# Optimization experiments

Hardware: AMD Instinct MI355X
Metric: run time of the kernel (lower is better)

The kernel has to match this reference:

```python
import jax, jax.numpy as jnp
import numpy as np


def setup_inputs() -> dict:
    key = jax.random.key(0)
    kx, ks = jax.random.split(key)
    X = jax.random.normal(kx, (8, 4096, 16), dtype=jnp.float32)
    # nn.Parameter(torch.rand(1) + 1.0)
    sigma = jax.random.uniform(ks, (1,), dtype=jnp.float32) + 1.0
    return {"X": X, "sigma": sigma}


def reference(X, sigma):
    sq = jnp.sum(X * X, axis=-1)                       # [B, N]
    inner = jnp.einsum('bnf,bmf->bnm', X, X)           # [B, N, N]
    sqdist = sq[:, :, None] + sq[:, None, :] - 2.0 * inner
    sqdist = jnp.maximum(sqdist, 0.0)                  # guard tiny negatives
    gaussian = jnp.exp(-sqdist / sigma[0])             # [B, N, N]
    # original _softmax: exp(gaussian) / sum over dim 2 == softmax over axis 2
    return jax.nn.softmax(gaussian, axis=2)
```

## Files before the change

kernel.cpp:

```cpp
#include <hip/hip_runtime.h>


constexpr int Bn  = 8;
constexpr int N   = 4096;
constexpr int F   = 16;
constexpr int TN  = 4;
constexpr int BLK = 256;
constexpr int WPB = BLK / 64;
constexpr int GROUPS = (N / 4) / BLK;

__global__ __launch_bounds__(256)
void pack_kernel(const float* __restrict__ X, float* __restrict__ Xt) {
    const int b = blockIdx.y;
    const int m = blockIdx.x * 256 + threadIdx.x;
    const float4* src = (const float4*)(X + ((size_t)b * N + m) * F);
    const float4 v0 = src[0], v1 = src[1], v2 = src[2], v3 = src[3];
    const float x[F] = {v0.x, v0.y, v0.z, v0.w, v1.x, v1.y, v1.z, v1.w,
                        v2.x, v2.y, v2.z, v2.w, v3.x, v3.y, v3.z, v3.w};
    float* dst = Xt + (size_t)b * F * N + m;
    #pragma unroll
    for (int f = 0; f < F; ++f) dst[(size_t)f * N] = x[f];
}

__device__ __forceinline__ float uni(float x) {
    return __int_as_float(__builtin_amdgcn_readfirstlane(__float_as_int(x)));
}

__device__ __forceinline__ float gse(float d, float base, float nis) {
    float sqd = fmaxf(fmaf(-2.0f, d, base), 0.0f);
    return __expf(__expf(sqd * nis));
}

template <bool WRITE>
__global__ __launch_bounds__(BLK)
__attribute__((amdgpu_waves_per_eu(2, 4)))
void gs_pass(const float* __restrict__ X, const float* __restrict__ Xt,
             const float* __restrict__ sigma_p, float* __restrict__ invsum,
             float* __restrict__ out) {
    __shared__ float red[TN][WPB];

    const int tid = threadIdx.x;
    const int b   = blockIdx.y;
    const int n0  = blockIdx.x * TN;
    const float* Xb = X + (size_t)b * N * F;

    float q[TN][F];
    float sqn[TN];
    #pragma unroll
    for (int r = 0; r < TN; ++r) {
        float s = 0.f;
        #pragma unroll
        for (int f = 0; f < F; ++f) {
            const float qq = uni(Xb[(size_t)(n0 + r) * F + f]);
            q[r][f] = qq;
            s = fmaf(qq, qq, s);
        }
        sqn[r] = uni(s);
    }
    const float nis = uni(-1.0f / sigma_p[0]);

    float inv[TN];
    if (WRITE) {
        #pragma unroll
        for (int r = 0; r < TN; ++r) inv[r] = uni(invsum[(size_t)b * N + n0 + r]);
    }

    const float4* Xt4 = (const float4*)(Xt + (size_t)b * F * N);
    float sums[TN] = {0.f, 0.f, 0.f, 0.f};

    #pragma unroll 1
    for (int g = 0; g < GROUPS; ++g) {
        const int c4 = g * BLK + tid;

        float4 d[TN];
        #pragma unroll
        for (int r = 0; r < TN; ++r) d[r] = make_float4(0.f, 0.f, 0.f, 0.f);
        float4 sq = make_float4(0.f, 0.f, 0.f, 0.f);

        #pragma unroll
        for (int fb = 0; fb < F / 4; ++fb) {
            float4 v0 = Xt4[(size_t)(fb * 4 + 0) * (N / 4) + c4];
            float4 v1 = Xt4[(size_t)(fb * 4 + 1) * (N / 4) + c4];
            float4 v2 = Xt4[(size_t)(fb * 4 + 2) * (N / 4) + c4];
            float4 v3 = Xt4[(size_t)(fb * 4 + 3) * (N / 4) + c4];

            #pragma unroll
            for (int k = 0; k < 4; ++k) {
                const float4 w = (k == 0) ? v0 : (k == 1) ? v1 : (k == 2) ? v2 : v3;
                sq.x = fmaf(w.x, w.x, sq.x);
                sq.y = fmaf(w.y, w.y, sq.y);
                sq.z = fmaf(w.z, w.z, sq.z);
                sq.w = fmaf(w.w, w.w, sq.w);
                #pragma unroll
                for (int r = 0; r < TN; ++r) {
                    const float qf = q[r][fb * 4 + k];
                    d[r].x = fmaf(qf, w.x, d[r].x);
                    d[r].y = fmaf(qf, w.y, d[r].y);
                    d[r].z = fmaf(qf, w.z, d[r].z);
                    d[r].w = fmaf(qf, w.w, d[r].w);
                }
            }
        }

        #pragma unroll
        for (int r = 0; r < TN; ++r) {
            float4 e;
            e.x = gse(d[r].x, sqn[r] + sq.x, nis);
            e.y = gse(d[r].y, sqn[r] + sq.y, nis);
            e.z = gse(d[r].z, sqn[r] + sq.z, nis);
            e.w = gse(d[r].w, sqn[r] + sq.w, nis);
            if (WRITE) {
                float4 o = make_float4(e.x * inv[r], e.y * inv[r],
                                       e.z * inv[r], e.w * inv[r]);
                ((float4*)(out + ((size_t)b * N + n0 + r) * N))[c4] = o;
            } else {
                sums[r] += (e.x + e.y) + (e.z + e.w);
            }
        }
    }

    if (!WRITE) {
        #pragma unroll
        for (int r = 0; r < TN; ++r) {
            float s = sums[r];
            #pragma unroll
            for (int off = 32; off > 0; off >>= 1) s += __shfl_down(s, off, 64);
            if ((tid & 63) == 0) red[r][tid >> 6] = s;
        }
        __syncthreads();
        if (tid < TN) {
            float t = 0.f;
            #pragma unroll
            for (int w = 0; w < WPB; ++w) t += red[tid][w];
            invsum[(size_t)b * N + n0 + tid] = 1.0f / t;
        }
    }
}

extern "C" void kernel_launch(void* const* d_in, const int* in_sizes, int n_in,
                              void* d_out, int out_size, void* d_ws, size_t ws_size,
                              hipStream_t stream) {
    const float* X     = (const float*)d_in[0];
    const float* sigma = (const float*)d_in[1];
    float* out         = (float*)d_out;
    float* Xt          = (float*)d_ws;
    float* invsum      = (float*)d_ws + (size_t)Bn * F * N;

    pack_kernel<<<dim3(N / 256, Bn), 256, 0, stream>>>(X, Xt);
    gs_pass<false><<<dim3(N / TN, Bn), BLK, 0, stream>>>(X, Xt, sigma, invsum, out);
    gs_pass<true ><<<dim3(N / TN, Bn), BLK, 0, stream>>>(X, Xt, sigma, invsum, out);
}
```

Before: 666.8 us.

## Fuse two softmax passes into one kernel keeping row values in registers

Replaces the two-pass approach (sum pass, then recompute-and-write pass) with a single kernel. With 512 threads, each thread holds GROUPS=2 x TN=4 float4 exp values in registers, block-reduces the row sums, then scales and writes the results. Column squared norms are now computed once in the pack kernel and loaded, instead of being recomputed per tile. This halves the distance and double-exp computation at the cost of more register pressure and a block-wide sync before any stores.

Result: slower. 1.462 ms (+119.3%).

```diff
diff --git a/kernel.cpp b/kernel.cpp
--- a/kernel.cpp
+++ b/kernel.cpp
@@ -5,12 +5,13 @@
 constexpr int N   = 4096;
 constexpr int F   = 16;
 constexpr int TN  = 4;
-constexpr int BLK = 256;
+constexpr int BLK = 512;
 constexpr int WPB = BLK / 64;
 constexpr int GROUPS = (N / 4) / BLK;
 
 __global__ __launch_bounds__(256)
-void pack_kernel(const float* __restrict__ X, float* __restrict__ Xt) {
+void pack_kernel(const float* __restrict__ X, float* __restrict__ Xt,
+                 float* __restrict__ sqm) {
     const int b = blockIdx.y;
     const int m = blockIdx.x * 256 + threadIdx.x;
     const float4* src = (const float4*)(X + ((size_t)b * N + m) * F);
@@ -18,8 +19,13 @@
     const float x[F] = {v0.x, v0.y, v0.z, v0.w, v1.x, v1.y, v1.z, v1.w,
                         v2.x, v2.y, v2.z, v2.w, v3.x, v3.y, v3.z, v3.w};
     float* dst = Xt + (size_t)b * F * N + m;
+    float s = 0.f;
     #pragma unroll
-    for (int f = 0; f < F; ++f) dst[(size_t)f * N] = x[f];
+    for (int f = 0; f < F; ++f) {
+        dst[(size_t)f * N] = x[f];
+        s = fmaf(x[f], x[f], s);
+    }
+    sqm[(size_t)b * N + m] = s;
 }
 
 __device__ __forceinline__ float uni(float x) {
@@ -31,12 +37,10 @@
     return __expf(__expf(sqd * nis));
 }
 
-template <bool WRITE>
-__global__ __launch_bounds__(BLK)
-__attribute__((amdgpu_waves_per_eu(2, 4)))
-void gs_pass(const float* __restrict__ X, const float* __restrict__ Xt,
-             const float* __restrict__ sigma_p, float* __restrict__ invsum,
-             float* __restrict__ out) {
+__global__ __launch_bounds__(BLK, 4)
+void gs_single(const float* __restrict__ X, const float* __restrict__ Xt,
+               const float* __restrict__ sqm, const float* __restrict__ sigma_p,
+               float* __restrict__ out) {
     __shared__ float red[TN][WPB];
 
     const int tid = threadIdx.x;
@@ -59,23 +63,19 @@
     }
     const float nis = uni(-1.0f / sigma_p[0]);
 
-    float inv[TN];
-    if (WRITE) {
-        #pragma unroll
-        for (int r = 0; r < TN; ++r) inv[r] = uni(invsum[(size_t)b * N + n0 + r]);
-    }
+    const float4* Xt4  = (const float4*)(Xt + (size_t)b * F * N);
+    const float4* sqm4 = (const float4*)(sqm + (size_t)b * N);
 
-    const float4* Xt4 = (const float4*)(Xt + (size_t)b * F * N);
-    float sums[TN] = {0.f, 0.f, 0.f, 0.f};
+    float4 e[GROUPS][TN];
+    float  sums[TN] = {0.f, 0.f, 0.f, 0.f};
 
-    #pragma unroll 1
+    #pragma unroll
     for (int g = 0; g < GROUPS; ++g) {
         const int c4 = g * BLK + tid;
 
         float4 d[TN];
         #pragma unroll
         for (int r = 0; r < TN; ++r) d[r] = make_float4(0.f, 0.f, 0.f, 0.f);
-        float4 sq = make_float4(0.f, 0.f, 0.f, 0.f);
 
         #pragma unroll
         for (int fb = 0; fb < F / 4; ++fb) {
@@ -87,10 +87,6 @@
             #pragma unroll
             for (int k = 0; k < 4; ++k) {
                 const float4 w = (k == 0) ? v0 : (k == 1) ? v1 : (k == 2) ? v2 : v3;
-                sq.x = fmaf(w.x, w.x, sq.x);
-                sq.y = fmaf(w.y, w.y, sq.y);
-                sq.z = fmaf(w.z, w.z, sq.z);
-                sq.w = fmaf(w.w, w.w, sq.w);
                 #pragma unroll
                 for (int r = 0; r < TN; ++r) {
                     const float qf = q[r][fb * 4 + k];
@@ -102,37 +98,47 @@
             }
         }
 
+        const float4 sm = sqm4[c4];
+
         #pragma unroll
         for (int r = 0; r < TN; ++r) {
-            float4 e;
-            e.x = gse(d[r].x, sqn[r] + sq.x, nis);
-            e.y = gse(d[r].y, sqn[r] + sq.y, nis);
-            e.z = gse(d[r].z, sqn[r] + sq.z, nis);
-            e.w = gse(d[r].w, sqn[r] + sq.w, nis);
-            if (WRITE) {
-                float4 o = make_float4(e.x * inv[r], e.y * inv[r],
-                                       e.z * inv[r], e.w * inv[r]);
-                ((float4*)(out + ((size_t)b * N + n0 + r) * N))[c4] = o;
-            } else {
-                sums[r] += (e.x + e.y) + (e.z + e.w);
-            }
+            float4 ee;
+            ee.x = gse(d[r].x, sqn[r] + sm.x, nis);
+            ee.y = gse(d[r].y, sqn[r] + sm.y, nis);
+            ee.z = gse(d[r].z, sqn[r] + sm.z, nis);
+            ee.w = gse(d[r].w, sqn[r] + sm.w, nis);
+            e[g][r] = ee;
+            sums[r] += (ee.x + ee.y) + (ee.z + ee.w);
         }
     }
 
-    if (!WRITE) {
+    #pragma unroll
+    for (int r = 0; r < TN; ++r) {
+        float s = sums[r];
+        #pragma unroll
+        for (int off = 32; off > 0; off >>= 1) s += __shfl_down(s, off, 64);
+        if ((tid & 63) == 0) red[r][tid >> 6] = s;
+    }
+    __syncthreads();
+
+    float inv[TN];
+    #pragma unroll
+    for (int r = 0; r < TN; ++r) {
+        float t = 0.f;
+        #pragma unroll
+        for (int w = 0; w < WPB; ++w) t += red[r][w];
+        inv[r] = 1.0f / t;
+    }
+
+    float* outb = out + ((size_t)b * N + n0) * (size_t)N;
+    #pragma unroll
+    for (int g = 0; g < GROUPS; ++g) {
+        const int c4 = g * BLK + tid;
         #pragma unroll
         for (int r = 0; r < TN; ++r) {
-            float s = sums[r];
-            #pragma unroll
-            for (int off = 32; off > 0; off >>= 1) s += __shfl_down(s, off, 64);
-            if ((tid & 63) == 0) red[r][tid >> 6] = s;
-        }
-        __syncthreads();
-        if (tid < TN) {
-            float t = 0.f;
-            #pragma unroll
-            for (int w = 0; w < WPB; ++w) t += red[tid][w];
-            invsum[(size_t)b * N + n0 + tid] = 1.0f / t;
+            float4 v = e[g][r];
+            v.x *= inv[r]; v.y *= inv[r]; v.z *= inv[r]; v.w *= inv[r];
+            ((float4*)(outb + (size_t)r * N))[c4] = v;
         }
     }
 }
@@ -144,9 +150,8 @@
     const float* sigma = (const float*)d_in[1];
     float* out         = (float*)d_out;
     float* Xt          = (float*)d_ws;
-    float* invsum      = (float*)d_ws + (size_t)Bn * F * N;
+    float* sqm         = (float*)d_ws + (size_t)Bn * F * N;
 
-    pack_kernel<<<dim3(N / 256, Bn), 256, 0, stream>>>(X, Xt);
-    gs_pass<false><<<dim3(N / TN, Bn), BLK, 0, stream>>>(X, Xt, sigma, invsum, out);
-    gs_pass<true ><<<dim3(N / TN, Bn), BLK, 0, stream>>>(X, Xt, sigma, invsum, out);
+    pack_kernel<<<dim3(N / 256, Bn), 256, 0, stream>>>(X, Xt, sqm);
+    gs_single<<<dim3(N / TN, Bn), BLK, 0, stream>>>(X, Xt, sqm, sigma, out);
 }
```
